# Performance work log

Measured on AMD Instinct MI355X. Metric: run time of the kernel, lower is better.

The kernel has to match this reference:

```python
import jax, jax.numpy as jnp
import numpy as np

B, N, K, DEG = 128, 4096, 25, 16
BN_EPS = 1e-5


def setup_inputs() -> dict:
    key = jax.random.key(0)
    ks = jax.random.split(key, 16)

    def sp_lap(k, V):
        # fixed-degree random sparse scaled Laplacian (COO); values scaled so the
        # K=25 Chebyshev recursion x2 = 2*L@x1 - x0 stays numerically bounded
        rows = jnp.repeat(jnp.arange(V, dtype=jnp.int32), DEG)
        cols = jax.random.randint(k, (V * DEG,), 0, V, dtype=jnp.int32)
        vals = jax.random.normal(jax.random.fold_in(k, 1), (V * DEG,), jnp.float32) * 0.05
        return rows, cols, vals

    l0_rows, l0_cols, l0_vals = sp_lap(ks[0], N)
    l2_rows, l2_cols, l2_vals = sp_lap(ks[1], N // 4)
    l4_rows, l4_cols, l4_vals = sp_lap(ks[2], N // 16)

    x = jax.random.normal(ks[3], (B, N, 1), jnp.float32)
    w1 = jax.random.normal(ks[4], (1 * K, 32), jnp.float32) * 0.1
    b1 = jnp.zeros((32,), jnp.float32)
    w2 = jax.random.normal(ks[5], (32 * K, 64), jnp.float32) * 0.05
    b2 = jnp.zeros((64,), jnp.float32)
    w3 = jax.random.normal(ks[6], (64 * K, 64), jnp.float32) * 0.05
    b3 = jnp.zeros((64,), jnp.float32)
    fc1_w = jax.random.normal(ks[7], (N // 16 * 64, 512), jnp.float32) * 0.01
    fc1_b = jnp.zeros((512,), jnp.float32)
    bn_gamma = jnp.ones((512,), jnp.float32)
    bn_beta = jnp.zeros((512,), jnp.float32)
    fc2_w = jax.random.normal(ks[8], (512, 10), jnp.float32) * 0.05
    fc2_b = jnp.zeros((10,), jnp.float32)

    return dict(x=x,
                l0_rows=l0_rows, l0_cols=l0_cols, l0_vals=l0_vals,
                l2_rows=l2_rows, l2_cols=l2_cols, l2_vals=l2_vals,
                l4_rows=l4_rows, l4_cols=l4_cols, l4_vals=l4_vals,
                w1=w1, b1=b1, w2=w2, b2=b2, w3=w3, b3=b3,
                fc1_w=fc1_w, fc1_b=fc1_b, bn_gamma=bn_gamma, bn_beta=bn_beta,
                fc2_w=fc2_w, fc2_b=fc2_b)


def spmm(rows, cols, vals, xm, V):
    # sparse (V,V) @ dense (V,M) via gather + segment-sum
    return jax.ops.segment_sum(vals[:, None] * xm[cols], rows, num_segments=V)


def cheb(rows, cols, vals, x, W, b):
    # GCNCheb: Chebyshev polynomial basis T_k(L) x, k=0..K-1, then linear projection
    Bb, V, Fin = x.shape
    Kk = W.shape[0] // Fin
    x0 = jnp.transpose(x, (1, 2, 0)).reshape(V, Fin * Bb)  # (V, Fin*B)
    xs = [x0]
    x1 = spmm(rows, cols, vals, x0, V)
    xs.append(x1)
    for _ in range(2, Kk):
        x2 = 2.0 * spmm(rows, cols, vals, x1, V) - x0
        xs.append(x2)
        x0, x1 = x1, x2
    Xc = jnp.stack(xs, 0).reshape(Kk, V, Fin, Bb)          # (K, V, Fin, B)
    Xc = jnp.transpose(Xc, (3, 1, 2, 0)).reshape(Bb * V, Fin * Kk)
    return (Xc @ W + b).reshape(Bb, V, -1)


def pool4(x):
    # max-pool over consecutive groups of 4 nodes (gcn_pool_4)
    Bb, V, F = x.shape
    return x.reshape(Bb, V // 4, 4, F).max(axis=2)


def reference(x,
              l0_rows, l0_cols, l0_vals,
              l2_rows, l2_cols, l2_vals,
              l4_rows, l4_cols, l4_vals,
              w1, b1, w2, b2, w3, b3,
              fc1_w, fc1_b, bn_gamma, bn_beta, fc2_w, fc2_b):
    h = jax.nn.relu(cheb(l0_rows, l0_cols, l0_vals, x, w1, b1))
    h = pool4(h)                                             # (B, N/4, 32)
    h = jax.nn.relu(cheb(l2_rows, l2_cols, l2_vals, h, w2, b2))
    h = pool4(h)                                             # (B, N/16, 64)
    h = jax.nn.relu(cheb(l4_rows, l4_cols, l4_vals, h, w3, b3))
    h = h.reshape(h.shape[0], -1)                            # (B, N/16 * 64)
    h = h @ fc1_w + fc1_b                                    # (B, 512)
    mean = h.mean(axis=0)
    var = h.var(axis=0)  # biased, matching torch BatchNorm training normalization
    h = (h - mean) / jnp.sqrt(var + BN_EPS) * bn_gamma + bn_beta
    h = jax.nn.relu(h)
    logits = h @ fc2_w + fc2_b                               # (B, 10)
    return jax.nn.log_softmax(logits, axis=1)
```

## Files before the change

### kernel.cpp

```cpp
#include <hip/hip_runtime.h>

#define B_ 128
#define K_ 25
#define DEG_ 16

#define R4(X) X(0) X(1) X(2) X(3)

typedef __attribute__((ext_vector_type(4))) float f32x4;
typedef __attribute__((ext_vector_type(8))) short bf16x8;

__device__ __forceinline__ float4 f4ma(float t, float4 w, float4 a) {
    a.x = fmaf(t, w.x, a.x); a.y = fmaf(t, w.y, a.y);
    a.z = fmaf(t, w.z, a.z); a.w = fmaf(t, w.w, a.w);
    return a;
}
__device__ __forceinline__ float4 f4max(float4 a, float4 b) {
    return make_float4(fmaxf(a.x, b.x), fmaxf(a.y, b.y), fmaxf(a.z, b.z), fmaxf(a.w, b.w));
}
__device__ __forceinline__ float4 f4sub2(float4 s, float4 p) {
    return make_float4(2.f * s.x - p.x, 2.f * s.y - p.y, 2.f * s.z - p.z, 2.f * s.w - p.w);
}
__device__ __forceinline__ unsigned f2bfu(float f) {
    unsigned u = __float_as_uint(f);
    return (u + 0x7FFFu + ((u >> 16) & 1u)) >> 16;
}
__device__ __forceinline__ unsigned packbf(float e, float o) { return f2bfu(e) | (f2bfu(o) << 16); }

__device__ __forceinline__ bf16x8 u2b(uint4 u) {
    union { uint4 u4; bf16x8 b8; } c; c.u4 = u; return c.b8;
}
__device__ __forceinline__ f32x4 mfma_bf(uint4 a, uint4 b, f32x4 c) {
    return __builtin_amdgcn_mfma_f32_16x16x32_bf16(u2b(a), u2b(b), c, 0, 0, 0);
}


__global__ __launch_bounds__(256) void k_transpose_x(const float* __restrict__ x, float* __restrict__ x0) {
    int i = blockIdx.x * 256 + threadIdx.x;
    int v = i >> 7, b = i & 127;
    x0[i] = x[(b << 12) + v];
}

__global__ __launch_bounds__(256) void k_packw(const float* __restrict__ w2, const float* __restrict__ w3,
        unsigned short* __restrict__ wb2, unsigned short* __restrict__ wb3) {
    int i = blockIdx.x * 256 + threadIdx.x;
    if (i < 51200) {
        int k = i >> 11, rem = i & 2047, fo = rem >> 5, fi = rem & 31;
        wb2[i] = (unsigned short)f2bfu(w2[(size_t)(fi * K_ + k) * 64 + fo]);
    }
    if (i < 102400) {
        int k = i >> 12, rem = i & 4095, fo = rem >> 6, fi = rem & 63;
        wb3[i] = (unsigned short)f2bfu(w3[(size_t)(fi * K_ + k) * 64 + fo]);
    }
}

__global__ __launch_bounds__(256) void k_spmm1(const int* __restrict__ cols, const float* __restrict__ vals,
        const float2* __restrict__ cur, const float2* __restrict__ prev,
        float2* __restrict__ next, int two) {
    int t = blockIdx.x * 256 + threadIdx.x;
    int v = __builtin_amdgcn_readfirstlane(t >> 6);
    int lane = threadIdx.x & 63;
    int base = v * DEG_;
    float2 s = make_float2(0.f, 0.f);
#pragma unroll
    for (int d = 0; d < DEG_; ++d) {
        float wv = vals[base + d];
        float2 xx = cur[((size_t)cols[base + d] << 6) + lane];
        s.x = fmaf(wv, xx.x, s.x); s.y = fmaf(wv, xx.y, s.y);
    }
    size_t idx = ((size_t)v << 6) + lane;
    if (two) {
        float2 p = prev[idx];
        s.x = 2.f * s.x - p.x; s.y = 2.f * s.y - p.y;
    }
    next[idx] = s;
}

__global__ __launch_bounds__(256) void k_chain2(const int* __restrict__ cols, const float* __restrict__ vals,
        float* __restrict__ stA, float* __restrict__ stB, unsigned* __restrict__ mir,
        int k0, int nsteps) {
    __shared__ float st[2][8192];
    int s = blockIdx.x, t = threadIdx.x;
    size_t sb = (size_t)s * 8192;
#pragma unroll
    for (int r = 0; r < 4; ++r) {
        int v = t + (r << 8);
        *(float4*)&st[0][v*8]     = *(const float4*)(stA + sb + v*8);
        *(float4*)&st[0][v*8 + 4] = *(const float4*)(stA + sb + v*8 + 4);
        *(float4*)&st[1][v*8]     = *(const float4*)(stB + sb + v*8);
        *(float4*)&st[1][v*8 + 4] = *(const float4*)(stB + sb + v*8 + 4);
    }
    __syncthreads();
    int pc = 0, pb = 1;
    for (int step = 0; step < nsteps; ++step) {
        int k = k0 + step;
        float4 n0_0, n1_0, n0_1, n1_1, n0_2, n1_2, n0_3, n1_3;
#define C2_CMP(r, N0, N1) { \
        int v = t + (r << 8); \
        const int4* cp = (const int4*)(cols + v * 16); \
        const float4* vp = (const float4*)(vals + v * 16); \
        float4 a0 = make_float4(0.f,0.f,0.f,0.f), a1 = a0; \
        for (int dd = 0; dd < 4; ++dd) { \
            int4 cc = cp[dd]; float4 ww = vp[dd]; \
            const float* p; \
            p = &st[pc][cc.x * 8]; a0 = f4ma(ww.x, *(const float4*)p, a0); a1 = f4ma(ww.x, *(const float4*)(p+4), a1); \
            p = &st[pc][cc.y * 8]; a0 = f4ma(ww.y, *(const float4*)p, a0); a1 = f4ma(ww.y, *(const float4*)(p+4), a1); \
            p = &st[pc][cc.z * 8]; a0 = f4ma(ww.z, *(const float4*)p, a0); a1 = f4ma(ww.z, *(const float4*)(p+4), a1); \
            p = &st[pc][cc.w * 8]; a0 = f4ma(ww.w, *(const float4*)p, a0); a1 = f4ma(ww.w, *(const float4*)(p+4), a1); \
        } \
        if (k >= 2) { \
            float4 p0 = *(const float4*)&st[pb][v*8], p1 = *(const float4*)&st[pb][v*8+4]; \
            a0 = f4sub2(a0, p0); a1 = f4sub2(a1, p1); \
        } \
        N0 = a0; N1 = a1; }
        C2_CMP(0, n0_0, n1_0)
        C2_CMP(1, n0_1, n1_1)
        C2_CMP(2, n0_2, n1_2)
        C2_CMP(3, n0_3, n1_3)
#undef C2_CMP
        __syncthreads();
        unsigned* ms = mir + (size_t)(k % 5) * 2097152 + (size_t)s * 4096;
#define C2_ST(r, N0, N1) { \
        int v = t + (r << 8); \
        *(float4*)&st[pb][v*8] = N0; *(float4*)&st[pb][v*8+4] = N1; \
        uint4 mw = make_uint4(packbf(N0.x, N1.x), packbf(N0.y, N1.y), packbf(N0.z, N1.z), packbf(N0.w, N1.w)); \
        *(uint4*)(ms + v * 4) = mw; }
        C2_ST(0, n0_0, n1_0)
        C2_ST(1, n0_1, n1_1)
        C2_ST(2, n0_2, n1_2)
        C2_ST(3, n0_3, n1_3)
#undef C2_ST
        __syncthreads();
        int tmp = pc; pc = pb; pb = tmp;
    }
#pragma unroll
    for (int r = 0; r < 4; ++r) {
        int v = t + (r << 8);
        *(float4*)(stA + sb + v*8)     = *(const float4*)&st[pc][v*8];
        *(float4*)(stA + sb + v*8 + 4) = *(const float4*)&st[pc][v*8+4];
        *(float4*)(stB + sb + v*8)     = *(const float4*)&st[pb][v*8];
        *(float4*)(stB + sb + v*8 + 4) = *(const float4*)&st[pb][v*8+4];
    }
}

__global__ __launch_bounds__(512) void k_chain3(const int* __restrict__ cols, const float* __restrict__ vals,
        float* __restrict__ stA, float* __restrict__ stB, unsigned* __restrict__ mir,
        int k0, int nsteps) {
    __shared__ float st[2][8192];
    int s = blockIdx.x, t = threadIdx.x;
    int v = t >> 1, h = t & 1;
    int o0 = v * 32 + h * 8;
    size_t sb = (size_t)s * 8192;
    *(float4*)&st[0][o0]      = *(const float4*)(stA + sb + o0);
    *(float4*)&st[0][o0 + 4]  = *(const float4*)(stA + sb + o0 + 4);
    *(float4*)&st[0][o0 + 16] = *(const float4*)(stA + sb + o0 + 16);
    *(float4*)&st[0][o0 + 20] = *(const float4*)(stA + sb + o0 + 20);
    *(float4*)&st[1][o0]      = *(const float4*)(stB + sb + o0);
    *(float4*)&st[1][o0 + 4]  = *(const float4*)(stB + sb + o0 + 4);
    *(float4*)&st[1][o0 + 16] = *(const float4*)(stB + sb + o0 + 16);
    *(float4*)&st[1][o0 + 20] = *(const float4*)(stB + sb + o0 + 20);
    __syncthreads();
    int pc = 0, pb = 1;
    const int4* cp = (const int4*)(cols + v * 16);
    const float4* vp = (const float4*)(vals + v * 16);
    for (int step = 0; step < nsteps; ++step) {
        int k = k0 + step;
        float4 ae0 = make_float4(0.f,0.f,0.f,0.f), ae1 = ae0, ao0 = ae0, ao1 = ae0;
        for (int dd = 0; dd < 4; ++dd) {
            int4 cc = cp[dd]; float4 ww = vp[dd];
            const float* p;
            p = &st[pc][cc.x * 32 + h * 8];
            ae0 = f4ma(ww.x, *(const float4*)p, ae0);       ae1 = f4ma(ww.x, *(const float4*)(p+4), ae1);
            ao0 = f4ma(ww.x, *(const float4*)(p+16), ao0);  ao1 = f4ma(ww.x, *(const float4*)(p+20), ao1);
            p = &st[pc][cc.y * 32 + h * 8];
            ae0 = f4ma(ww.y, *(const float4*)p, ae0);       ae1 = f4ma(ww.y, *(const float4*)(p+4), ae1);
            ao0 = f4ma(ww.y, *(const float4*)(p+16), ao0);  ao1 = f4ma(ww.y, *(const float4*)(p+20), ao1);
            p = &st[pc][cc.z * 32 + h * 8];
            ae0 = f4ma(ww.z, *(const float4*)p, ae0);       ae1 = f4ma(ww.z, *(const float4*)(p+4), ae1);
            ao0 = f4ma(ww.z, *(const float4*)(p+16), ao0);  ao1 = f4ma(ww.z, *(const float4*)(p+20), ao1);
            p = &st[pc][cc.w * 32 + h * 8];
            ae0 = f4ma(ww.w, *(const float4*)p, ae0);       ae1 = f4ma(ww.w, *(const float4*)(p+4), ae1);
            ao0 = f4ma(ww.w, *(const float4*)(p+16), ao0);  ao1 = f4ma(ww.w, *(const float4*)(p+20), ao1);
        }
        if (k >= 2) {
            ae0 = f4sub2(ae0, *(const float4*)&st[pb][o0]);
            ae1 = f4sub2(ae1, *(const float4*)&st[pb][o0 + 4]);
            ao0 = f4sub2(ao0, *(const float4*)&st[pb][o0 + 16]);
            ao1 = f4sub2(ao1, *(const float4*)&st[pb][o0 + 20]);
        }
        __syncthreads();
        *(float4*)&st[pb][o0]      = ae0;
        *(float4*)&st[pb][o0 + 4]  = ae1;
        *(float4*)&st[pb][o0 + 16] = ao0;
        *(float4*)&st[pb][o0 + 20] = ao1;
        unsigned* ms = mir + (size_t)(k % 5) * 1048576 + (size_t)s * 4096 + v * 16 + h * 8;
        uint4 w0 = make_uint4(packbf(ae0.x, ao0.x), packbf(ae0.y, ao0.y), packbf(ae0.z, ao0.z), packbf(ae0.w, ao0.w));
        uint4 w1 = make_uint4(packbf(ae1.x, ao1.x), packbf(ae1.y, ao1.y), packbf(ae1.z, ao1.z), packbf(ae1.w, ao1.w));
        *(uint4*)(ms) = w0;
        *(uint4*)(ms + 4) = w1;
        __syncthreads();
        int tmp = pc; pc = pb; pb = tmp;
    }
    *(float4*)(stA + sb + o0)      = *(const float4*)&st[pc][o0];
    *(float4*)(stA + sb + o0 + 4)  = *(const float4*)&st[pc][o0 + 4];
    *(float4*)(stA + sb + o0 + 16) = *(const float4*)&st[pc][o0 + 16];
    *(float4*)(stA + sb + o0 + 20) = *(const float4*)&st[pc][o0 + 20];
    *(float4*)(stB + sb + o0)      = *(const float4*)&st[pb][o0];
    *(float4*)(stB + sb + o0 + 4)  = *(const float4*)&st[pb][o0 + 4];
    *(float4*)(stB + sb + o0 + 16) = *(const float4*)&st[pb][o0 + 16];
    *(float4*)(stB + sb + o0 + 20) = *(const float4*)&st[pb][o0 + 20];
}

__global__ __launch_bounds__(256) void k_proj1_pool(const float* __restrict__ basis,
        const float* __restrict__ W1, const float* __restrict__ b1, float* __restrict__ st2,
        unsigned* __restrict__ mir) {
    int half = blockIdx.y;
    int i = blockIdx.x * 256 + threadIdx.x;
    int g = i >> 7, b = i & 127;
    const float* wbase = W1 + half * 16;
#define P1_DM(j) float4 M##j = make_float4(-1e30f, -1e30f, -1e30f, -1e30f);
    R4(P1_DM)
#undef P1_DM
    for (int r = 0; r < 4; ++r) {
        const float* bp = basis + (((size_t)(4 * g + r) << 7) + b);
#define P1_DC(j) float4 C##j = make_float4(0.f, 0.f, 0.f, 0.f);
        R4(P1_DC)
#undef P1_DC
#pragma unroll 5
        for (int k = 0; k < K_; ++k) {
            float tv = bp[(size_t)k * 524288];
            const float4* w = (const float4*)(wbase + k * 32);
#define P1_FM(j) C##j = f4ma(tv, w[j], C##j);
            R4(P1_FM)
#undef P1_FM
        }
#define P1_MX(j) M##j = f4max(M##j, C##j);
        R4(P1_MX)
#undef P1_MX
    }
    const float* bb = b1 + half * 16;
    int bq = b >> 2, bo = b & 3;
#define P1_ST(j) { \
    float e0 = fmaxf(M##j.x + bb[4*j+0], 0.f); \
    float o0 = fmaxf(M##j.y + bb[4*j+1], 0.f); \
    float e1 = fmaxf(M##j.z + bb[4*j+2], 0.f); \
    float o1 = fmaxf(M##j.w + bb[4*j+3], 0.f); \
    int f2a = half * 8 + 2 * j; \
    float* sa = st2 + ((size_t)(f2a * 32 + bq)) * 8192 + g * 8 + bo; \
    float* sbp = st2 + ((size_t)((f2a + 1) * 32 + bq)) * 8192 + g * 8 + bo; \
    sa[0] = e0; sa[4] = o0; sbp[0] = e1; sbp[4] = o1; \
    mir[((size_t)(f2a * 32 + bq)) * 4096 + g * 4 + bo] = packbf(e0, o0); \
    mir[((size_t)((f2a + 1) * 32 + bq)) * 4096 + g * 4 + bo] = packbf(e1, o1); }
    R4(P1_ST)
#undef P1_ST
}

__global__ __launch_bounds__(256) void k_proj_l2m(const unsigned* __restrict__ mir, size_t slotH,
        const uint4* __restrict__ wb, float* __restrict__ acc, int k0, int init,
        const float* __restrict__ bias) {
    int wid = blockIdx.x * 4 + (threadIdx.x >> 6);
    int lane = threadIdx.x & 63;
    int lm = lane & 15, lg = lane >> 4;
    int v = wid >> 3, b0 = (wid & 7) << 4;
    float* ap = acc + ((size_t)v << 13) + b0 + (lg << 2);
    f32x4 C0, C1, C2, C3;
    if (init) {
        float q0 = bias[lm], q1 = bias[16 + lm], q2 = bias[32 + lm], q3 = bias[48 + lm];
        C0 = f32x4{q0, q0, q0, q0}; C1 = f32x4{q1, q1, q1, q1};
        C2 = f32x4{q2, q2, q2, q2}; C3 = f32x4{q3, q3, q3, q3};
    } else {
        C0 = *(const f32x4*)(ap + (size_t)lm * 128);
        C1 = *(const f32x4*)(ap + (size_t)(16 + lm) * 128);
        C2 = *(const f32x4*)(ap + (size_t)(32 + lm) * 128);
        C3 = *(const f32x4*)(ap + (size_t)(48 + lm) * 128);
    }
    int b = b0 + lm;
    const unsigned* mp0 = mir + ((size_t)((lg << 2) * 32 + (b >> 2))) * 4096 + (size_t)v * 4 + (b & 3);
#pragma unroll
    for (int kk = 0; kk < 5; ++kk) {
        const unsigned* mp = mp0 + (size_t)kk * slotH;
        uint4 a = make_uint4(mp[0], mp[131072], mp[262144], mp[393216]);
        int kb = (k0 + kk) << 6;
        uint4 w0 = wb[(kb + lm) * 4 + lg];
        uint4 w1 = wb[(kb + 16 + lm) * 4 + lg];
        uint4 w2 = wb[(kb + 32 + lm) * 4 + lg];
        uint4 w3 = wb[(kb + 48 + lm) * 4 + lg];
        C0 = mfma_bf(a, w0, C0);
        C1 = mfma_bf(a, w1, C1);
        C2 = mfma_bf(a, w2, C2);
        C3 = mfma_bf(a, w3, C3);
    }
    *(f32x4*)(ap + (size_t)lm * 128) = C0;
    *(f32x4*)(ap + (size_t)(16 + lm) * 128) = C1;
    *(f32x4*)(ap + (size_t)(32 + lm) * 128) = C2;
    *(f32x4*)(ap + (size_t)(48 + lm) * 128) = C3;
}

__global__ __launch_bounds__(256) void k_proj_l3m(const unsigned* __restrict__ mir, size_t slotH,
        const uint4* __restrict__ wb, float* __restrict__ acc, int k0, int init,
        const float* __restrict__ bias, int finalrelu) {
    int wid = blockIdx.x * 4 + (threadIdx.x >> 6);
    int lane = threadIdx.x & 63;
    int lm = lane & 15, lg = lane >> 4;
    int v = wid >> 3, b0 = (wid & 7) << 4;
    float* ap = acc + ((size_t)v << 13) + b0 + (lg << 2);
    f32x4 C0, C1, C2, C3;
    if (init) {
        float q0 = bias[lm], q1 = bias[16 + lm], q2 = bias[32 + lm], q3 = bias[48 + lm];
        C0 = f32x4{q0, q0, q0, q0}; C1 = f32x4{q1, q1, q1, q1};
        C2 = f32x4{q2, q2, q2, q2}; C3 = f32x4{q3, q3, q3, q3};
    } else {
        C0 = *(const f32x4*)(ap + (size_t)lm * 128);
        C1 = *(const f32x4*)(ap + (size_t)(16 + lm) * 128);
        C2 = *(const f32x4*)(ap + (size_t)(32 + lm) * 128);
        C3 = *(const f32x4*)(ap + (size_t)(48 + lm) * 128);
    }
    int bq4 = wid & 7;
    const unsigned* mp0 = mir + (size_t)v * 16 + lm;
#pragma unroll
    for (int kk = 0; kk < 5; ++kk) {
        const unsigned* mpk = mp0 + (size_t)kk * slotH;
        int kb = (k0 + kk) << 6;
#pragma unroll
        for (int ks = 0; ks < 2; ++ks) {
            const unsigned* mk = mpk + ((size_t)(((ks << 4) + (lg << 2)) * 8 + bq4)) * 4096;
            uint4 a = make_uint4(mk[0], mk[32768], mk[65536], mk[98304]);
            int wof = (ks << 2) + lg;
            uint4 w0 = wb[(kb + lm) * 8 + wof];
            uint4 w1 = wb[(kb + 16 + lm) * 8 + wof];
            uint4 w2 = wb[(kb + 32 + lm) * 8 + wof];
            uint4 w3 = wb[(kb + 48 + lm) * 8 + wof];
            C0 = mfma_bf(a, w0, C0);
            C1 = mfma_bf(a, w1, C1);
            C2 = mfma_bf(a, w2, C2);
            C3 = mfma_bf(a, w3, C3);
        }
    }
    if (finalrelu) {
#pragma unroll
        for (int r = 0; r < 4; ++r) {
            C0[r] = fmaxf(C0[r], 0.f); C1[r] = fmaxf(C1[r], 0.f);
            C2[r] = fmaxf(C2[r], 0.f); C3[r] = fmaxf(C3[r], 0.f);
        }
    }
    *(f32x4*)(ap + (size_t)lm * 128) = C0;
    *(f32x4*)(ap + (size_t)(16 + lm) * 128) = C1;
    *(f32x4*)(ap + (size_t)(32 + lm) * 128) = C2;
    *(f32x4*)(ap + (size_t)(48 + lm) * 128) = C3;
}

__global__ __launch_bounds__(256) void k_relu_pool_m(const float* __restrict__ acc,
        float* __restrict__ st3, unsigned* __restrict__ mir) {
    int i = blockIdx.x * 256 + threadIdx.x;
    int g = i >> 12, fi2 = (i >> 7) & 31, b = i & 127;
    const float* ap = acc + (((size_t)g << 2) << 13) + (fi2 << 8) + b;
    float me = 0.f, mo = 0.f;
#pragma unroll
    for (int r = 0; r < 4; ++r) {
        me = fmaxf(me, ap[0]); mo = fmaxf(mo, ap[128]);
        ap += 8192;
    }
    int s = fi2 * 8 + (b >> 4), bo = b & 15;
    st3[(size_t)s * 8192 + g * 32 + bo] = me;
    st3[(size_t)s * 8192 + g * 32 + 16 + bo] = mo;
    mir[(size_t)s * 4096 + g * 16 + bo] = packbf(me, mo);
}

__global__ __launch_bounds__(256) void k_fc1_part(const float* __restrict__ t3, const float* __restrict__ w,
                           float* __restrict__ part) {
    int blk = blockIdx.x;
    int bg = blk >> 7;
    int rs = (blk >> 1) & 63;
    int j = ((blk & 1) << 8) + threadIdx.x;
    int b0 = bg << 3;
    float a0=0.f,a1=0.f,a2=0.f,a3=0.f,a4=0.f,a5=0.f,a6=0.f,a7=0.f;
    int r0 = rs << 8;
#pragma unroll 4
    for (int row = r0; row < r0 + 256; ++row) {
        float wv = w[((size_t)row << 9) + j];
        const float4* tp = (const float4*)(t3 + ((size_t)row << 7) + b0);
        float4 t0 = tp[0], t1 = tp[1];
        a0 = fmaf(t0.x, wv, a0);
        a1 = fmaf(t0.y, wv, a1);
        a2 = fmaf(t0.z, wv, a2);
        a3 = fmaf(t0.w, wv, a3);
        a4 = fmaf(t1.x, wv, a4);
        a5 = fmaf(t1.y, wv, a5);
        a6 = fmaf(t1.z, wv, a6);
        a7 = fmaf(t1.w, wv, a7);
    }
    float* pp = part + (((size_t)(rs << 7) + b0) << 9) + j;
    pp[0*512]=a0; pp[1*512]=a1; pp[2*512]=a2; pp[3*512]=a3;
    pp[4*512]=a4; pp[5*512]=a5; pp[6*512]=a6; pp[7*512]=a7;
}

__global__ __launch_bounds__(256) void k_fc1_red(const float* __restrict__ part, const float* __restrict__ bias,
                          float* __restrict__ h) {
    int i = blockIdx.x * 256 + threadIdx.x;
    float a = bias[i & 511];
#pragma unroll 8
    for (int rs = 0; rs < 64; ++rs) a += part[((size_t)rs << 16) + i];
    h[i] = a;
}

__global__ void k_bnstats(const float* __restrict__ h, float* __restrict__ mv) {
    __shared__ float s1[128], s2[128];
    int j = blockIdx.x, t = threadIdx.x;
    float v = h[(size_t)t * 512 + j];
    s1[t] = v; s2[t] = v * v;
    __syncthreads();
    for (int o = 64; o > 0; o >>= 1) {
        if (t < o) { s1[t] += s1[t + o]; s2[t] += s2[t + o]; }
        __syncthreads();
    }
    if (t == 0) {
        float m = s1[0] * (1.f / 128.f);
        float var = s2[0] * (1.f / 128.f) - m * m;
        mv[j] = m;
        mv[512 + j] = rsqrtf(var + 1e-5f);
    }
}

__global__ void k_head(const float* __restrict__ h, const float* __restrict__ mv,
                       const float* __restrict__ gamma, const float* __restrict__ beta,
                       const float* __restrict__ w2, const float* __restrict__ b2,
                       float* __restrict__ out) {
    __shared__ float hr[512];
    __shared__ float lg[16];
    int b = blockIdx.x, t = threadIdx.x;
    for (int j = t; j < 512; j += 64) {
        float x = (h[(size_t)b * 512 + j] - mv[j]) * mv[512 + j] * gamma[j] + beta[j];
        hr[j] = fmaxf(x, 0.f);
    }
    __syncthreads();
    if (t < 10) {
        float a = b2[t];
        for (int j = 0; j < 512; ++j) a += hr[j] * w2[j * 10 + t];
        lg[t] = a;
    }
    __syncthreads();
    if (t == 0) {
        float mx = -1e30f;
        for (int q = 0; q < 10; ++q) mx = fmaxf(mx, lg[q]);
        float sum = 0.f;
        for (int q = 0; q < 10; ++q) sum += expf(lg[q] - mx);
        float ls = logf(sum) + mx;
        for (int q = 0; q < 10; ++q) out[b * 10 + q] = lg[q] - ls;
    }
}

extern "C" void kernel_launch(void* const* d_in, const int* in_sizes, int n_in,
                              void* d_out, int out_size, void* d_ws, size_t ws_size,
                              hipStream_t stream) {
    (void)in_sizes; (void)n_in; (void)out_size; (void)ws_size;
    const float* x      = (const float*)d_in[0];
    const int*   l0cols = (const int*)d_in[2];
    const float* l0vals = (const float*)d_in[3];
    const int*   l2cols = (const int*)d_in[5];
    const float* l2vals = (const float*)d_in[6];
    const int*   l4cols = (const int*)d_in[8];
    const float* l4vals = (const float*)d_in[9];
    const float* w1   = (const float*)d_in[10];
    const float* b1   = (const float*)d_in[11];
    const float* w2   = (const float*)d_in[12];
    const float* b2   = (const float*)d_in[13];
    const float* w3   = (const float*)d_in[14];
    const float* b3   = (const float*)d_in[15];
    const float* fc1w = (const float*)d_in[16];
    const float* fc1b = (const float*)d_in[17];
    const float* gam  = (const float*)d_in[18];
    const float* bet  = (const float*)d_in[19];
    const float* fc2w = (const float*)d_in[20];
    const float* fc2b = (const float*)d_in[21];
    float* out = (float*)d_out;

    const size_t S1 = 4096 * 128;
    const size_t S2 = 1024 * 4096;
    const size_t S3 = 256 * 8192;

    float* ws = (float*)d_ws;
    float* basis1 = ws;
    float* st2A   = ws + 25 * S1;
    float* st2B   = st2A + S2;
    unsigned* mir2 = (unsigned*)(st2B + S2);
    float* acc3   = (float*)(mir2 + 5 * (S2 / 2));
    float* h      = acc3 + S3;
    float* mv     = h + 65536;
    unsigned short* wb2 = (unsigned short*)(mv + 1024);
    unsigned short* wb3 = wb2 + 51200;
    float* acc2   = basis1;
    float* st3A   = st2A;
    float* st3B   = st2B;
    unsigned* mir3 = mir2;
    float* part   = basis1;

    k_packw<<<400, 256, 0, stream>>>(w2, w3, wb2, wb3);

    k_transpose_x<<<2048, 256, 0, stream>>>(x, basis1);
    for (int k = 1; k < 25; ++k) {
        const float* cur  = basis1 + (size_t)(k - 1) * S1;
        const float* prev = (k >= 2) ? basis1 + (size_t)(k - 2) * S1 : cur;
        float* next = basis1 + (size_t)k * S1;
        k_spmm1<<<1024, 256, 0, stream>>>(l0cols, l0vals, (const float2*)cur,
                                          (const float2*)prev, (float2*)next, k >= 2 ? 1 : 0);
    }
    k_proj1_pool<<<dim3(512, 2), 256, 0, stream>>>(basis1, w1, b1, st2A, mir2);

    for (int c = 0; c < 5; ++c) {
        int kk0 = (c == 0) ? 1 : 5 * c;
        int ns  = (c == 0) ? 4 : 5;
        k_chain2<<<512, 256, 0, stream>>>(l2cols, l2vals, st2A, st2B, mir2, kk0, ns);
        k_proj_l2m<<<2048, 256, 0, stream>>>(mir2, S2 / 2, (const uint4*)wb2, acc2, 5 * c,
                                             c == 0 ? 1 : 0, b2);
    }
    k_relu_pool_m<<<4096, 256, 0, stream>>>(acc2, st3A, mir3);

    for (int c = 0; c < 5; ++c) {
        int kk0 = (c == 0) ? 1 : 5 * c;
        int ns  = (c == 0) ? 4 : 5;
        k_chain3<<<256, 512, 0, stream>>>(l4cols, l4vals, st3A, st3B, mir3, kk0, ns);
        k_proj_l3m<<<512, 256, 0, stream>>>(mir3, S3 / 2, (const uint4*)wb3, acc3, 5 * c,
                                            c == 0 ? 1 : 0, b3, c == 4 ? 1 : 0);
    }

    k_fc1_part<<<2048, 256, 0, stream>>>(acc3, fc1w, part);
    k_fc1_red<<<256, 256, 0, stream>>>(part, fc1b, h);
    k_bnstats<<<512, 128, 0, stream>>>(h, mv);
    k_head<<<128, 64, 0, stream>>>(h, mv, gam, bet, fc2w, fc2b, out);
}
```

Before: 959.1 us.

## Shrink Chebyshev chain slabs to 4 columns and keep previous term in registers

The layer-2 and layer-3 Chebyshev chain kernels now split the per-block state into narrower slabs of 4 feature/batch columns, using a stride-5 shared-memory layout to avoid bank conflicts. The previous Chebyshev term is held in registers instead of a second shared buffer. This cuts shared memory per block and raises block counts (512→1024 and 256→2048), aiming for more occupancy and parallelism. The pool, projection and relu-pool kernels have their state and mirror indexing rewritten to match the new slab layout. The cost is more blocks that each re-read the cols/vals arrays, giving more redundant index traffic.

```diff
diff --git a/kernel.cpp b/kernel.cpp
--- a/kernel.cpp
+++ b/kernel.cpp
@@ -78,136 +78,85 @@
 __global__ __launch_bounds__(256) void k_chain2(const int* __restrict__ cols, const float* __restrict__ vals,
         float* __restrict__ stA, float* __restrict__ stB, unsigned* __restrict__ mir,
         int k0, int nsteps) {
-    __shared__ float st[2][8192];
+    __shared__ float st[5120];
     int s = blockIdx.x, t = threadIdx.x;
-    size_t sb = (size_t)s * 8192;
-#pragma unroll
-    for (int r = 0; r < 4; ++r) {
-        int v = t + (r << 8);
-        *(float4*)&st[0][v*8]     = *(const float4*)(stA + sb + v*8);
-        *(float4*)&st[0][v*8 + 4] = *(const float4*)(stA + sb + v*8 + 4);
-        *(float4*)&st[1][v*8]     = *(const float4*)(stB + sb + v*8);
-        *(float4*)&st[1][v*8 + 4] = *(const float4*)(stB + sb + v*8 + 4);
-    }
+    size_t sb = (size_t)s * 4096;
+    float4 p0, p1, p2, p3;
+#define C2_LD(r, P) { int v = t + (r << 8); \
+    *(float4*)&st[v * 5] = *(const float4*)(stA + sb + v * 4); \
+    P = *(const float4*)(stB + sb + v * 4); }
+    C2_LD(0, p0) C2_LD(1, p1) C2_LD(2, p2) C2_LD(3, p3)
+#undef C2_LD
     __syncthreads();
-    int pc = 0, pb = 1;
+    float4 n0, n1, n2, n3;
     for (int step = 0; step < nsteps; ++step) {
         int k = k0 + step;
-        float4 n0_0, n1_0, n0_1, n1_1, n0_2, n1_2, n0_3, n1_3;
-#define C2_CMP(r, N0, N1) { \
-        int v = t + (r << 8); \
-        const int4* cp = (const int4*)(cols + v * 16); \
-        const float4* vp = (const float4*)(vals + v * 16); \
-        float4 a0 = make_float4(0.f,0.f,0.f,0.f), a1 = a0; \
-        for (int dd = 0; dd < 4; ++dd) { \
-            int4 cc = cp[dd]; float4 ww = vp[dd]; \
-            const float* p; \
-            p = &st[pc][cc.x * 8]; a0 = f4ma(ww.x, *(const float4*)p, a0); a1 = f4ma(ww.x, *(const float4*)(p+4), a1); \
-            p = &st[pc][cc.y * 8]; a0 = f4ma(ww.y, *(const float4*)p, a0); a1 = f4ma(ww.y, *(const float4*)(p+4), a1); \
-            p = &st[pc][cc.z * 8]; a0 = f4ma(ww.z, *(const float4*)p, a0); a1 = f4ma(ww.z, *(const float4*)(p+4), a1); \
-            p = &st[pc][cc.w * 8]; a0 = f4ma(ww.w, *(const float4*)p, a0); a1 = f4ma(ww.w, *(const float4*)(p+4), a1); \
-        } \
-        if (k >= 2) { \
-            float4 p0 = *(const float4*)&st[pb][v*8], p1 = *(const float4*)&st[pb][v*8+4]; \
-            a0 = f4sub2(a0, p0); a1 = f4sub2(a1, p1); \
-        } \
-        N0 = a0; N1 = a1; }
-        C2_CMP(0, n0_0, n1_0)
-        C2_CMP(1, n0_1, n1_1)
-        C2_CMP(2, n0_2, n1_2)
-        C2_CMP(3, n0_3, n1_3)
+        float4 c0, c1, c2, c3;
+#define C2_CMP(r, N, C, P) { int v = t + (r << 8); \
+    const int4* cp = (const int4*)(cols + v * 16); \
+    const float4* vp = (const float4*)(vals + v * 16); \
+    float4 a = make_float4(0.f, 0.f, 0.f, 0.f); \
+    for (int dd = 0; dd < 4; ++dd) { \
+        int4 cc = cp[dd]; float4 ww = vp[dd]; \
+        a = f4ma(ww.x, *(const float4*)&st[cc.x * 5], a); \
+        a = f4ma(ww.y, *(const float4*)&st[cc.y * 5], a); \
+        a = f4ma(ww.z, *(const float4*)&st[cc.z * 5], a); \
+        a = f4ma(ww.w, *(const float4*)&st[cc.w * 5], a); \
+    } \
+    C = *(const float4*)&st[v * 5]; \
+    N = (k >= 2) ? f4sub2(a, P) : a; }
+        C2_CMP(0, n0, c0, p0) C2_CMP(1, n1, c1, p1) C2_CMP(2, n2, c2, p2) C2_CMP(3, n3, c3, p3)
 #undef C2_CMP
         __syncthreads();
-        unsigned* ms = mir + (size_t)(k % 5) * 2097152 + (size_t)s * 4096;
-#define C2_ST(r, N0, N1) { \
-        int v = t + (r << 8); \
-        *(float4*)&st[pb][v*8] = N0; *(float4*)&st[pb][v*8+4] = N1; \
-        uint4 mw = make_uint4(packbf(N0.x, N1.x), packbf(N0.y, N1.y), packbf(N0.z, N1.z), packbf(N0.w, N1.w)); \
-        *(uint4*)(ms + v * 4) = mw; }
-        C2_ST(0, n0_0, n1_0)
-        C2_ST(1, n0_1, n1_1)
-        C2_ST(2, n0_2, n1_2)
-        C2_ST(3, n0_3, n1_3)
+        unsigned* ms = mir + (size_t)(k % 5) * 2097152 + (size_t)s * 2048;
+#define C2_ST(r, N, C, P) { int v = t + (r << 8); \
+    *(float4*)&st[v * 5] = N; \
+    *(uint2*)(ms + v * 2) = make_uint2(packbf(N.x, N.z), packbf(N.y, N.w)); \
+    P = C; }
+        C2_ST(0, n0, c0, p0) C2_ST(1, n1, c1, p1) C2_ST(2, n2, c2, p2) C2_ST(3, n3, c3, p3)
 #undef C2_ST
         __syncthreads();
-        int tmp = pc; pc = pb; pb = tmp;
-    }
-#pragma unroll
-    for (int r = 0; r < 4; ++r) {
-        int v = t + (r << 8);
-        *(float4*)(stA + sb + v*8)     = *(const float4*)&st[pc][v*8];
-        *(float4*)(stA + sb + v*8 + 4) = *(const float4*)&st[pc][v*8+4];
-        *(float4*)(stB + sb + v*8)     = *(const float4*)&st[pb][v*8];
-        *(float4*)(stB + sb + v*8 + 4) = *(const float4*)&st[pb][v*8+4];
-    }
-}
-
-__global__ __launch_bounds__(512) void k_chain3(const int* __restrict__ cols, const float* __restrict__ vals,
+    }
+#define C2_OUT(r, N, P) { int v = t + (r << 8); \
+    *(float4*)(stA + sb + v * 4) = N; \
+    *(float4*)(stB + sb + v * 4) = P; }
+    C2_OUT(0, n0, p0) C2_OUT(1, n1, p1) C2_OUT(2, n2, p2) C2_OUT(3, n3, p3)
+#undef C2_OUT
+}
+
+__global__ __launch_bounds__(256) void k_chain3(const int* __restrict__ cols, const float* __restrict__ vals,
         float* __restrict__ stA, float* __restrict__ stB, unsigned* __restrict__ mir,
         int k0, int nsteps) {
-    __shared__ float st[2][8192];
+    __shared__ float st[1280];
     int s = blockIdx.x, t = threadIdx.x;
-    int v = t >> 1, h = t & 1;
-    int o0 = v * 32 + h * 8;
-    size_t sb = (size_t)s * 8192;
-    *(float4*)&st[0][o0]      = *(const float4*)(stA + sb + o0);
-    *(float4*)&st[0][o0 + 4]  = *(const float4*)(stA + sb + o0 + 4);
-    *(float4*)&st[0][o0 + 16] = *(const float4*)(stA + sb + o0 + 16);
-    *(float4*)&st[0][o0 + 20] = *(const float4*)(stA + sb + o0 + 20);
-    *(float4*)&st[1][o0]      = *(const float4*)(stB + sb + o0);
-    *(float4*)&st[1][o0 + 4]  = *(const float4*)(stB + sb + o0 + 4);
-    *(float4*)&st[1][o0 + 16] = *(const float4*)(stB + sb + o0 + 16);
-    *(float4*)&st[1][o0 + 20] = *(const float4*)(stB + sb + o0 + 20);
+    size_t sb = (size_t)s * 1024;
+    *(float4*)&st[t * 5] = *(const float4*)(stA + sb + t * 4);
+    float4 pr = *(const float4*)(stB + sb + t * 4);
     __syncthreads();
-    int pc = 0, pb = 1;
-    const int4* cp = (const int4*)(cols + v * 16);
-    const float4* vp = (const float4*)(vals + v * 16);
+    const int4* cp = (const int4*)(cols + t * 16);
+    const float4* vp = (const float4*)(vals + t * 16);
+    float4 n;
     for (int step = 0; step < nsteps; ++step) {
         int k = k0 + step;
-        float4 ae0 = make_float4(0.f,0.f,0.f,0.f), ae1 = ae0, ao0 = ae0, ao1 = ae0;
+        float4 a = make_float4(0.f, 0.f, 0.f, 0.f);
         for (int dd = 0; dd < 4; ++dd) {
             int4 cc = cp[dd]; float4 ww = vp[dd];
-            const float* p;
-            p = &st[pc][cc.x * 32 + h * 8];
-            ae0 = f4ma(ww.x, *(const float4*)p, ae0);       ae1 = f4ma(ww.x, *(const float4*)(p+4), ae1);
-            ao0 = f4ma(ww.x, *(const float4*)(p+16), ao0);  ao1 = f4ma(ww.x, *(const float4*)(p+20), ao1);
-            p = &st[pc][cc.y * 32 + h * 8];
-            ae0 = f4ma(ww.y, *(const float4*)p, ae0);       ae1 = f4ma(ww.y, *(const float4*)(p+4), ae1);
-            ao0 = f4ma(ww.y, *(const float4*)(p+16), ao0);  ao1 = f4ma(ww.y, *(const float4*)(p+20), ao1);
-            p = &st[pc][cc.z * 32 + h * 8];
-            ae0 = f4ma(ww.z, *(const float4*)p, ae0);       ae1 = f4ma(ww.z, *(const float4*)(p+4), ae1);
-            ao0 = f4ma(ww.z, *(const float4*)(p+16), ao0);  ao1 = f4ma(ww.z, *(const float4*)(p+20), ao1);
-            p = &st[pc][cc.w * 32 + h * 8];
-            ae0 = f4ma(ww.w, *(const float4*)p, ae0);       ae1 = f4ma(ww.w, *(const float4*)(p+4), ae1);
-            ao0 = f4ma(ww.w, *(const float4*)(p+16), ao0);  ao1 = f4ma(ww.w, *(const float4*)(p+20), ao1);
+            a = f4ma(ww.x, *(const float4*)&st[cc.x * 5], a);
+            a = f4ma(ww.y, *(const float4*)&st[cc.y * 5], a);
+            a = f4ma(ww.z, *(const float4*)&st[cc.z * 5], a);
+            a = f4ma(ww.w, *(const float4*)&st[cc.w * 5], a);
         }
-        if (k >= 2) {
-            ae0 = f4sub2(ae0, *(const float4*)&st[pb][o0]);
-            ae1 = f4sub2(ae1, *(const float4*)&st[pb][o0 + 4]);
-            ao0 = f4sub2(ao0, *(const float4*)&st[pb][o0 + 16]);
-            ao1 = f4sub2(ao1, *(const float4*)&st[pb][o0 + 20]);
-        }
+        float4 c = *(const float4*)&st[t * 5];
+        n = (k >= 2) ? f4sub2(a, pr) : a;
         __syncthreads();
-        *(float4*)&st[pb][o0]      = ae0;
-        *(float4*)&st[pb][o0 + 4]  = ae1;
-        *(float4*)&st[pb][o0 + 16] = ao0;
-        *(float4*)&st[pb][o0 + 20] = ao1;
-        unsigned* ms = mir + (size_t)(k % 5) * 1048576 + (size_t)s * 4096 + v * 16 + h * 8;
-        uint4 w0 = make_uint4(packbf(ae0.x, ao0.x), packbf(ae0.y, ao0.y), packbf(ae0.z, ao0.z), packbf(ae0.w, ao0.w));
-        uint4 w1 = make_uint4(packbf(ae1.x, ao1.x), packbf(ae1.y, ao1.y), packbf(ae1.z, ao1.z), packbf(ae1.w, ao1.w));
-        *(uint4*)(ms) = w0;
-        *(uint4*)(ms + 4) = w1;
+        *(float4*)&st[t * 5] = n;
+        unsigned* ms = mir + (size_t)(k % 5) * 1048576 + (size_t)s * 512;
+        *(uint2*)(ms + t * 2) = make_uint2(packbf(n.x, n.z), packbf(n.y, n.w));
+        pr = c;
         __syncthreads();
-        int tmp = pc; pc = pb; pb = tmp;
-    }
-    *(float4*)(stA + sb + o0)      = *(const float4*)&st[pc][o0];
-    *(float4*)(stA + sb + o0 + 4)  = *(const float4*)&st[pc][o0 + 4];
-    *(float4*)(stA + sb + o0 + 16) = *(const float4*)&st[pc][o0 + 16];
-    *(float4*)(stA + sb + o0 + 20) = *(const float4*)&st[pc][o0 + 20];
-    *(float4*)(stB + sb + o0)      = *(const float4*)&st[pb][o0];
-    *(float4*)(stB + sb + o0 + 4)  = *(const float4*)&st[pb][o0 + 4];
-    *(float4*)(stB + sb + o0 + 16) = *(const float4*)&st[pb][o0 + 16];
-    *(float4*)(stB + sb + o0 + 20) = *(const float4*)&st[pb][o0 + 20];
+    }
+    *(float4*)(stA + sb + t * 4) = n;
+    *(float4*)(stB + sb + t * 4) = pr;
 }
 
 __global__ __launch_bounds__(256) void k_proj1_pool(const float* __restrict__ basis,
@@ -238,18 +187,19 @@
 #undef P1_MX
     }
     const float* bb = b1 + half * 16;
-    int bq = b >> 2, bo = b & 3;
+    int bh = b >> 1, bo = b & 1;
 #define P1_ST(j) { \
     float e0 = fmaxf(M##j.x + bb[4*j+0], 0.f); \
     float o0 = fmaxf(M##j.y + bb[4*j+1], 0.f); \
     float e1 = fmaxf(M##j.z + bb[4*j+2], 0.f); \
     float o1 = fmaxf(M##j.w + bb[4*j+3], 0.f); \
-    int f2a = half * 8 + 2 * j; \
-    float* sa = st2 + ((size_t)(f2a * 32 + bq)) * 8192 + g * 8 + bo; \
-    float* sbp = st2 + ((size_t)((f2a + 1) * 32 + bq)) * 8192 + g * 8 + bo; \
-    sa[0] = e0; sa[4] = o0; sbp[0] = e1; sbp[4] = o1; \
-    mir[((size_t)(f2a * 32 + bq)) * 4096 + g * 4 + bo] = packbf(e0, o0); \
-    mir[((size_t)((f2a + 1) * 32 + bq)) * 4096 + g * 4 + bo] = packbf(e1, o1); }
+    int s2a = (half * 8 + 2 * j) * 64 + bh; \
+    float* pa = st2 + (size_t)s2a * 4096 + g * 4 + bo; \
+    pa[0] = e0; pa[2] = o0; \
+    float* pb = st2 + (size_t)(s2a + 64) * 4096 + g * 4 + bo; \
+    pb[0] = e1; pb[2] = o1; \
+    mir[(size_t)s2a * 2048 + g * 2 + bo] = packbf(e0, o0); \
+    mir[(size_t)(s2a + 64) * 2048 + g * 2 + bo] = packbf(e1, o1); }
     R4(P1_ST)
 #undef P1_ST
 }
@@ -274,7 +224,7 @@
         C3 = *(const f32x4*)(ap + (size_t)(48 + lm) * 128);
     }
     int b = b0 + lm;
-    const unsigned* mp0 = mir + ((size_t)((lg << 2) * 32 + (b >> 2))) * 4096 + (size_t)v * 4 + (b & 3);
+    const unsigned* mp0 = mir + ((size_t)((lg << 2) * 64 + (b >> 1))) * 2048 + (v << 1) + (b & 1);
 #pragma unroll
     for (int kk = 0; kk < 5; ++kk) {
         const unsigned* mp = mp0 + (size_t)kk * slotH;
@@ -314,15 +264,15 @@
         C2 = *(const f32x4*)(ap + (size_t)(32 + lm) * 128);
         C3 = *(const f32x4*)(ap + (size_t)(48 + lm) * 128);
     }
-    int bq4 = wid & 7;
-    const unsigned* mp0 = mir + (size_t)v * 16 + lm;
+    int b = b0 + lm;
+    const unsigned* mp0 = mir + (size_t)(b >> 1) * 512 + (v << 1) + (b & 1);
 #pragma unroll
     for (int kk = 0; kk < 5; ++kk) {
         const unsigned* mpk = mp0 + (size_t)kk * slotH;
         int kb = (k0 + kk) << 6;
 #pragma unroll
         for (int ks = 0; ks < 2; ++ks) {
-            const unsigned* mk = mpk + ((size_t)(((ks << 4) + (lg << 2)) * 8 + bq4)) * 4096;
+            const unsigned* mk = mpk + (size_t)((ks << 4) + (lg << 2)) * 32768;
             uint4 a = make_uint4(mk[0], mk[32768], mk[65536], mk[98304]);
             int wof = (ks << 2) + lg;
             uint4 w0 = wb[(kb + lm) * 8 + wof];
@@ -359,10 +309,10 @@
         me = fmaxf(me, ap[0]); mo = fmaxf(mo, ap[128]);
         ap += 8192;
     }
-    int s = fi2 * 8 + (b >> 4), bo = b & 15;
-    st3[(size_t)s * 8192 + g * 32 + bo] = me;
-    st3[(size_t)s * 8192 + g * 32 + 16 + bo] = mo;
-    mir[(size_t)s * 4096 + g * 16 + bo] = packbf(me, mo);
+    int s3 = fi2 * 64 + (b >> 1), bo = b & 1;
+    st3[(size_t)s3 * 1024 + g * 4 + bo] = me;
+    st3[(size_t)s3 * 1024 + g * 4 + 2 + bo] = mo;
+    mir[(size_t)s3 * 512 + g * 2 + bo] = packbf(me, mo);
 }
 
 __global__ __launch_bounds__(256) void k_fc1_part(const float* __restrict__ t3, const float* __restrict__ w,
@@ -508,7 +458,7 @@
     for (int c = 0; c < 5; ++c) {
         int kk0 = (c == 0) ? 1 : 5 * c;
         int ns  = (c == 0) ? 4 : 5;
-        k_chain2<<<512, 256, 0, stream>>>(l2cols, l2vals, st2A, st2B, mir2, kk0, ns);
+        k_chain2<<<1024, 256, 0, stream>>>(l2cols, l2vals, st2A, st2B, mir2, kk0, ns);
         k_proj_l2m<<<2048, 256, 0, stream>>>(mir2, S2 / 2, (const uint4*)wb2, acc2, 5 * c,
                                              c == 0 ? 1 : 0, b2);
     }
@@ -517,7 +467,7 @@
     for (int c = 0; c < 5; ++c) {
         int kk0 = (c == 0) ? 1 : 5 * c;
         int ns  = (c == 0) ? 4 : 5;
-        k_chain3<<<256, 512, 0, stream>>>(l4cols, l4vals, st3A, st3B, mir3, kk0, ns);
+        k_chain3<<<2048, 256, 0, stream>>>(l4cols, l4vals, st3A, st3B, mir3, kk0, ns);
         k_proj_l3m<<<512, 256, 0, stream>>>(mir3, S3 / 2, (const uint4*)wb3, acc3, 5 * c,
                                             c == 0 ? 1 : 0, b3, c == 4 ? 1 : 0);
     }
```

Measured after the change: 1.156 ms. 20.5% more time.
